# Kernel optimization log

Hardware: AMD Instinct MI355X
Metric: run time of the kernel (lower is better)

Reference implementation:

```python
import jax, jax.numpy as jnp
import numpy as np


def _patch_desc(x, patch_size):
    # x: (n, c, h, w). Replicate-pad by patch_size//2 and gather all
    # patch_size*patch_size shifted views -> (n, c*p*p, h*w) descriptors.
    n, c, h, w = x.shape
    step = patch_size // 2
    y = jnp.pad(x, ((0, 0), (0, 0), (step, step), (step, step)), mode='edge')
    feats = [y[:, :, i:i + h, j:j + w]
             for i in range(patch_size) for j in range(patch_size)]
    d = jnp.stack(feats, axis=2)            # (n, c, p*p, h, w)
    return d.reshape(n, c * patch_size * patch_size, h * w)


def setup_inputs() -> dict:
    key = jax.random.key(0)
    k1, k2 = jax.random.split(key)
    n, c, h, w = 4, 16, 64, 64
    s = jax.random.normal(k1, (n, c, h, w), dtype=jnp.float32)
    t = jax.random.normal(k2, (n, c, h, w), dtype=jnp.float32)
    return {"s": s, "t": t, "patch_size": 3}


def reference(s, t, patch_size):
    n, c, h, w = s.shape
    q = _patch_desc(s, patch_size)          # (n, d, hw) source queries
    p = _patch_desc(t, patch_size)          # (n, d, hw) target points
    # Squared-L2 nearest neighbor per source patch (exact version of FLANN kNN)
    qn = jnp.sum(q * q, axis=1)             # (n, hw)
    pn = jnp.sum(p * p, axis=1)             # (n, hw)
    cross = jnp.einsum('ndi,ndj->nij', q, p)  # (n, hw_q, hw_t)
    d2 = qn[:, :, None] - 2.0 * cross + pn[:, None, :]
    idx = jnp.argmin(d2, axis=2)            # (n, hw) flat target index
    nnd = jnp.min(d2, axis=2)               # (n, hw) squared distance
    idy = idx // w
    idx_x = idx % w
    nnf = jnp.stack([idy.reshape(n, h, w), idx_x.reshape(n, h, w)], axis=1)
    nnd = nnd.reshape(n, 1, h, w)
    return nnf.astype(jnp.int32), nnd
```

## Files before the change

kernel.cpp:

```cpp
#include <hip/hip_runtime.h>


#define N_  4
#define C_  16
#define H_  64
#define W_  64
#define HW_ 4096
#define K_  160
#define SPLITS_M 4
#define KKSTRIDE 528

#define SPLITS_V 4
#define TILES_PER_SPLIT_V 4

typedef _Float16 f16;
typedef _Float16 f16x8 __attribute__((ext_vector_type(8)));
typedef float    f32x4 __attribute__((ext_vector_type(4)));
typedef float    f32x16 __attribute__((ext_vector_type(16)));

__device__ __forceinline__ int iclamp(int v, int lo, int hi) {
    return v < lo ? lo : (v > hi ? hi : v);
}

__device__ __forceinline__ void async_ld16(const void* g, void* l) {
    __builtin_amdgcn_global_load_lds(
        (const __attribute__((address_space(1))) unsigned int*)g,
        (__attribute__((address_space(3))) unsigned int*)l, 16, 0, 0);
}

__global__ __launch_bounds__(256)
void build_desc_norms_kernel(const float* __restrict__ s,
                             const float* __restrict__ t,
                             f16* __restrict__ Qh, f16* __restrict__ Ql,
                             f16* __restrict__ Ph, f16* __restrict__ Pl,
                             float* __restrict__ pn,
                             float* __restrict__ qn) {
    const int y0  = blockIdx.x;
    const int n   = blockIdx.y;
    const int src = blockIdx.z;
    const float* img = (src ? s : t) + n * (C_ * HW_);
    f16* Dh = src ? Qh : Ph;
    f16* Dl = src ? Ql : Pl;
    float* nrm = src ? qn : pn;

    __shared__ float imgS[3][C_][W_];
    __shared__ float nS[4][W_];
    const int tid = threadIdx.x;
    #pragma unroll
    for (int k = 0; k < 12; ++k) {
        const int idx = tid + k * 256;
        const int x = idx & 63, c = (idx >> 6) & 15, r = idx >> 10;
        const int gy = iclamp(y0 + r - 1, 0, H_ - 1);
        imgS[r][c][x] = img[c * HW_ + gy * W_ + x];
    }
    __syncthreads();

    const int q = tid >> 6, x = tid & 63;
    const int pix = y0 * W_ + x;
    float nacc = 0.f;
    #pragma unroll
    for (int u = 0; u < 5; ++u) {
        const int kk = q * 5 + u;
        if (kk < 18) {
            f16x8 hv, lv;
            const int d  = kk >> 1;
            const int c0 = (kk & 1) * 8;
            const int dy = (d * 11) >> 5;
            const int dx = d - dy * 3;
            const int xs = iclamp(x + dx - 1, 0, W_ - 1);
            #pragma unroll
            for (int cc = 0; cc < 8; ++cc) {
                const float v = imgS[dy][c0 + cc][xs];
                const f16 h = (f16)v;
                hv[cc] = h;
                lv[cc] = (f16)(v - (float)h);
                nacc += v * v;
            }
            const size_t off = ((size_t)(n * 20 + kk) * HW_ + pix) * 8;
            *(f16x8*)&Dh[off] = hv;
            *(f16x8*)&Dl[off] = lv;
        }
    }
    nS[q][x] = nacc;
    __syncthreads();
    if (tid < W_)
        nrm[n * HW_ + pix] = nS[0][tid] + nS[1][tid] + nS[2][tid] + nS[3][tid];
}

__global__ __launch_bounds__(256, 2)
void mfma_nn_kernel(const f16* __restrict__ Qh, const f16* __restrict__ Ql,
                    const f16* __restrict__ Ph, const f16* __restrict__ Pl,
                    const float* __restrict__ pn_g,
                    unsigned long long* __restrict__ partial) {
    const int bid   = blockIdx.x;
    const int split = bid & 3;
    const int n     = (bid >> 2) & 3;
    const int iblk  = bid >> 4;
    const int tid  = threadIdx.x;
    const int wave = tid >> 6, lane = tid & 63;
    const int col  = lane & 31;
    const int half = lane >> 5;
    const int irow0 = iblk * 128 + wave * 32;

    __shared__ f16 B0[18 * KKSTRIDE];
    __shared__ f16 B1[18 * KKSTRIDE];
    __shared__ f16 B2[18 * KKSTRIDE];
    __shared__ float pnS[1024];

    f16x8 Ah[9], Al[9];
    #pragma unroll
    for (int c = 0; c < 9; ++c) {
        const size_t off = ((size_t)(n * 20 + 2 * c + half) * HW_ +
                            irow0 + col) * 8;
        Ah[c] = *(const f16x8*)(Qh + off);
        Al[c] = *(const f16x8*)(Ql + off);
    }

    const int jsplit0 = split * 1024;
    #pragma unroll
    for (int k = 0; k < 4; ++k)
        pnS[tid + k * 256] = pn_g[n * HW_ + jsplit0 + tid + k * 256];

    float    bd[16];
    unsigned bj[16];
    #pragma unroll
    for (int r = 0; r < 16; ++r) { bd[r] = -3.0e38f; bj[r] = 0u; }

    const int nst = (wave < 2) ? 5 : 4;
    const int kk0 = (wave < 2) ? wave * 5 : 10 + (wave - 2) * 4;
    const f16* sbase = half ? Pl : Ph;

    #define STAGE(BUF, T)                                                     \
        {   _Pragma("unroll")                                                 \
            for (int u = 0; u < 5; ++u) {                                     \
                if (u < nst) {                                                \
                    const int kk = kk0 + u;                                   \
                    const f16* g = sbase + ((size_t)(n * 20 + kk) * HW_ +     \
                                            jsplit0 + (T) * 32 + col) * 8;    \
                    async_ld16(g, (void*)&BUF[kk * KKSTRIDE + lane * 8]);     \
                }                                                             \
            }                                                                 \
        }

    #define TWAIT()                                                           \
        {   if (wave < 2) asm volatile("s_waitcnt vmcnt(5)" ::: "memory");    \
            else          asm volatile("s_waitcnt vmcnt(4)" ::: "memory");    \
            asm volatile("s_barrier" ::: "memory");                           \
        }

    #define COMPUTE(BUF, T)                                                   \
        {   const float pnv = -0.5f * pnS[(T) * 32 + col];                    \
            f32x16 Cf;                                                        \
            _Pragma("unroll")                                                 \
            for (int r = 0; r < 16; ++r) Cf[r] = pnv;                         \
            __builtin_amdgcn_s_setprio(1);                                    \
            _Pragma("unroll")                                                 \
            for (int c = 0; c < 9; ++c) {                                     \
                const int kb = (2 * c + half) * KKSTRIDE + col * 8;           \
                const f16x8 bh = *(const f16x8*)&BUF[kb];                     \
                const f16x8 bl = *(const f16x8*)&BUF[kb + 256];               \
                Cf = __builtin_amdgcn_mfma_f32_32x32x16_f16(                  \
                    Ah[c], bh, Cf, 0, 0, 0);                                  \
                Cf = __builtin_amdgcn_mfma_f32_32x32x16_f16(                  \
                    Al[c], bh, Cf, 0, 0, 0);                                  \
                Cf = __builtin_amdgcn_mfma_f32_32x32x16_f16(                  \
                    Ah[c], bl, Cf, 0, 0, 0);                                  \
            }                                                                 \
            __builtin_amdgcn_s_setprio(0);                                    \
            const unsigned jloc = (unsigned)((T) * 32 + col);                 \
            _Pragma("unroll")                                                 \
            for (int r = 0; r < 16; ++r)                                      \
                if (Cf[r] > bd[r]) { bd[r] = Cf[r]; bj[r] = jloc; }           \
        }

    STAGE(B0, 0)
    STAGE(B1, 1)
    __syncthreads();

    for (int g = 0; g < 10; ++g) {
        const int t = g * 3;
        TWAIT()
        STAGE(B2, t + 2)
        COMPUTE(B0, t)
        TWAIT()
        STAGE(B0, t + 3)
        COMPUTE(B1, t + 1)
        TWAIT()
        STAGE(B1, t + 4)
        COMPUTE(B2, t + 2)
    }
    TWAIT()
    COMPUTE(B0, 30)
    asm volatile("s_waitcnt vmcnt(0)" ::: "memory");
    asm volatile("s_barrier" ::: "memory");
    COMPUTE(B1, 31)
    #undef STAGE
    #undef TWAIT
    #undef COMPUTE

    #pragma unroll
    for (int r = 0; r < 16; ++r) {
        float    d = bd[r];
        unsigned j = (unsigned)jsplit0 + bj[r];
        #pragma unroll
        for (int off = 1; off < 32; off <<= 1) {
            const float    od = __shfl_xor(d, off, 64);
            const unsigned oj = __shfl_xor(j, off, 64);
            const bool take = (od > d) || (od == d && oj < j);
            d = take ? od : d;
            j = take ? oj : j;
        }
        if (col == 0) {
            const int i = irow0 + (r & 3) + 8 * (r >> 2) + 4 * half;
            partial[(size_t)(split * N_ + n) * HW_ + i] =
                ((unsigned long long)j << 32) |
                (unsigned long long)__float_as_uint(-2.f * d);
        }
    }
}

__global__ __launch_bounds__(256)
void finalize_mfma_kernel(const unsigned long long* __restrict__ partial,
                          const float* __restrict__ qn_g,
                          float* __restrict__ out) {
    const int id  = blockIdx.x * 256 + threadIdx.x;
    const int n   = id >> 12;
    const int pix = id & 4095;
    float    bd = 3.0e38f;
    unsigned bj = 0u;
    #pragma unroll
    for (int sp = 0; sp < SPLITS_M; ++sp) {
        const unsigned long long v = partial[(size_t)(sp * N_ + n) * HW_ + pix];
        const float    d = __uint_as_float((unsigned)(v & 0xffffffffull));
        const unsigned j = (unsigned)(v >> 32);
        const bool take = (d < bd) || (d == bd && j < bj);
        bd = take ? d : bd;
        bj = take ? j : bj;
    }
    out[n * 2 * HW_ + pix]            = (float)(bj >> 6);
    out[n * 2 * HW_ + HW_ + pix]      = (float)(bj & 63);
    out[N_ * 2 * HW_ + n * HW_ + pix] = bd + qn_g[n * HW_ + pix];
}

__global__ __launch_bounds__(256)
void prep_norms_kernel(const float* __restrict__ s,
                       const float* __restrict__ t,
                       float* __restrict__ pn,
                       float* __restrict__ qn) {
    const int gid   = blockIdx.x * 256 + threadIdx.x;
    const int which = gid >> 14;
    const int id    = gid & 16383;
    const int n     = id >> 12;
    const int pix   = id & 4095;
    const int y = pix >> 6, x = pix & 63;
    const float* base = (which ? s : t) + n * (C_ * HW_);
    float acc = 0.f;
    for (int c = 0; c < C_; ++c) {
        const float* bc = base + c * HW_;
        #pragma unroll
        for (int dy = 0; dy < 3; ++dy) {
            const float* br = bc + iclamp(y + dy - 1, 0, H_ - 1) * W_;
            #pragma unroll
            for (int dx = 0; dx < 3; ++dx) {
                float v = br[iclamp(x + dx - 1, 0, W_ - 1)];
                acc += v * v;
            }
        }
    }
    (which ? qn : pn)[id] = acc;
}

__global__ __launch_bounds__(256)
void patchmatch_main_kernel(const float* __restrict__ s,
                            const float* __restrict__ t,
                            const float* __restrict__ pn_g,
                            const float* __restrict__ qn_g,
                            unsigned long long* __restrict__ partial) {
    const int yq    = blockIdx.x;
    const int n     = blockIdx.y;
    const int split = blockIdx.z;
    const int tid  = threadIdx.x;
    const int tx   = tid & 15;
    const int ty   = tid >> 4;
    const int i0   = ty * 4;
    const int jrow = tx >> 2;
    const int jx0  = (tx & 3) * 16;

    __shared__ float qS[C_][3][68];
    __shared__ float tS[C_][6][68];
    __shared__ float qnS[W_];

    const float* sb = s + n * (C_ * HW_);
    const float* tb = t + n * (C_ * HW_);

    #pragma unroll
    for (int k = 0; k < 3; ++k) {
        const int id = tid + k * 256;
        const int sg = id & 15;
        const int c  = (id >> 4) & 15;
        const int r  = id >> 8;
        const int gr = iclamp(yq + r - 1, 0, H_ - 1);
        const float4 v = *(const float4*)&sb[c * HW_ + gr * W_ + sg * 4];
        float* dst = &qS[c][r][1 + sg * 4];
        dst[0] = v.x; dst[1] = v.y; dst[2] = v.z; dst[3] = v.w;
    }
    if (tid < 48) {
        const int c  = tid & 15;
        const int r  = tid >> 4;
        const int gr = iclamp(yq + r - 1, 0, H_ - 1);
        qS[c][r][0]  = sb[c * HW_ + gr * W_];
        qS[c][r][65] = sb[c * HW_ + gr * W_ + 63];
    }
    if (tid < W_) qnS[tid] = qn_g[n * HW_ + yq * W_ + tid];

    unsigned long long best[4] = {~0ull, ~0ull, ~0ull, ~0ull};

    for (int ytl = 0; ytl < TILES_PER_SPLIT_V; ++ytl) {
        const int yt = split * TILES_PER_SPLIT_V + ytl;
        __syncthreads();
        #pragma unroll
        for (int k = 0; k < 6; ++k) {
            const int id = tid + k * 256;
            const int sg = id & 15;
            const int c  = (id >> 4) & 15;
            const int r  = id >> 8;
            const int gr = iclamp(4 * yt + r - 1, 0, H_ - 1);
            const float4 v = *(const float4*)&tb[c * HW_ + gr * W_ + sg * 4];
            float* dst = &tS[c][r][1 + sg * 4];
            dst[0] = v.x; dst[1] = v.y; dst[2] = v.z; dst[3] = v.w;
        }
        if (tid < 96) {
            const int c  = tid & 15;
            const int r  = tid >> 4;
            const int gr = iclamp(4 * yt + r - 1, 0, H_ - 1);
            tS[c][r][0]  = tb[c * HW_ + gr * W_];
            tS[c][r][65] = tb[c * HW_ + gr * W_ + 63];
        }
        __syncthreads();

        float acc[4][16];
        #pragma unroll
        for (int a = 0; a < 4; ++a)
            #pragma unroll
            for (int b = 0; b < 16; ++b) acc[a][b] = 0.f;

        for (int c = 0; c < C_; ++c) {
            #pragma unroll
            for (int dy = 0; dy < 3; ++dy) {
                float qv[6], tv[18];
                *(float4*)&qv[0] = *(const float4*)&qS[c][dy][i0];
                *(float2*)&qv[4] = *(const float2*)&qS[c][dy][i0 + 4];
                const float* trow = &tS[c][jrow + dy][jx0];
                *(float4*)&tv[0]  = *(const float4*)&trow[0];
                *(float4*)&tv[4]  = *(const float4*)&trow[4];
                *(float4*)&tv[8]  = *(const float4*)&trow[8];
                *(float4*)&tv[12] = *(const float4*)&trow[12];
                *(float2*)&tv[16] = *(const float2*)&trow[16];
                #pragma unroll
                for (int dx = 0; dx < 3; ++dx)
                    #pragma unroll
                    for (int a = 0; a < 4; ++a)
                        #pragma unroll
                        for (int b = 0; b < 16; ++b)
                            acc[a][b] += qv[a + dx] * tv[b + dx];
            }
        }

        const int jbase = yt * 256 + jrow * W_ + jx0;
        float pnv[16];
        const float* png = &pn_g[n * HW_ + jbase];
        *(float4*)&pnv[0]  = *(const float4*)&png[0];
        *(float4*)&pnv[4]  = *(const float4*)&png[4];
        *(float4*)&pnv[8]  = *(const float4*)&png[8];
        *(float4*)&pnv[12] = *(const float4*)&png[12];
        #pragma unroll
        for (int a = 0; a < 4; ++a) {
            const float qn = qnS[i0 + a];
            #pragma unroll
            for (int b = 0; b < 16; ++b) {
                const float d2 = qn + pnv[b] - 2.f * acc[a][b];
                unsigned long long cand =
                    ((unsigned long long)__float_as_uint(d2) << 32) |
                    (unsigned)(jbase + b);
                best[a] = cand < best[a] ? cand : best[a];
            }
        }
    }

    #pragma unroll
    for (int a = 0; a < 4; ++a) {
        unsigned long long v = best[a];
        #pragma unroll
        for (int mm = 8; mm >= 1; mm >>= 1) {
            unsigned long long o = __shfl_xor(v, mm, 64);
            v = o < v ? o : v;
        }
        best[a] = v;
    }
    if (tx == 0) {
        #pragma unroll
        for (int a = 0; a < 4; ++a)
            partial[((split * N_ + n) * HW_) + yq * W_ + i0 + a] = best[a];
    }
}

__global__ __launch_bounds__(256)
void finalize_kernel(const unsigned long long* __restrict__ partial,
                     float* __restrict__ out) {
    const int id  = blockIdx.x * 256 + threadIdx.x;
    const int n   = id >> 12;
    const int pix = id & 4095;
    unsigned long long best = ~0ull;
    #pragma unroll
    for (int sp = 0; sp < SPLITS_V; ++sp) {
        unsigned long long v = partial[(sp * N_ + n) * HW_ + pix];
        best = v < best ? v : best;
    }
    const unsigned j = (unsigned)(best & 0xffffffffu);
    const float d2 = __uint_as_float((unsigned)(best >> 32));
    out[n * 2 * HW_ + pix]            = (float)(j >> 6);
    out[n * 2 * HW_ + HW_ + pix]      = (float)(j & 63);
    out[N_ * 2 * HW_ + n * HW_ + pix] = d2;
}

__global__ __launch_bounds__(256)
void patchmatch_mono_kernel(const float* __restrict__ s,
                            const float* __restrict__ t,
                            float* __restrict__ out) {
    const int yq  = blockIdx.x;
    const int n   = blockIdx.y;
    const int tid = threadIdx.x;
    const int tx  = tid & 15;
    const int ty  = tid >> 4;
    const int i0  = ty * 4;
    const int jrow = tx >> 3;
    const int jx0  = (tx & 7) * 8;

    __shared__ float qS[C_][3][68];
    __shared__ float tS[C_][4][68];
    __shared__ float pnS[HW_];
    __shared__ float qnS[W_];

    const float* sb = s + n * (C_ * HW_);
    const float* tb = t + n * (C_ * HW_);

    for (int jj = tid; jj < HW_; jj += 256) {
        const int y = jj >> 6, x = jj & 63;
        float acc = 0.f;
        for (int c = 0; c < C_; ++c) {
            const float* tc = tb + c * HW_;
            #pragma unroll
            for (int dy = 0; dy < 3; ++dy) {
                const float* tr = tc + iclamp(y + dy - 1, 0, H_ - 1) * W_;
                #pragma unroll
                for (int dx = 0; dx < 3; ++dx) {
                    float v = tr[iclamp(x + dx - 1, 0, W_ - 1)];
                    acc += v * v;
                }
            }
        }
        pnS[jj] = acc;
    }
    for (int idx = tid; idx < C_ * 3 * 66; idx += 256) {
        const int c   = idx / (3 * 66);
        const int rem = idx - c * (3 * 66);
        const int rr  = rem / 66;
        const int xi  = rem - rr * 66;
        qS[c][rr][xi] = sb[c * HW_ + iclamp(yq + rr - 1, 0, H_ - 1) * W_ +
                           iclamp(xi - 1, 0, W_ - 1)];
    }
    __syncthreads();
    if (tid < W_) {
        float acc = 0.f;
        for (int c = 0; c < C_; ++c)
            #pragma unroll
            for (int dy = 0; dy < 3; ++dy)
                #pragma unroll
                for (int dx = 0; dx < 3; ++dx) {
                    float v = qS[c][dy][tid + dx];
                    acc += v * v;
                }
        qnS[tid] = acc;
    }

    unsigned long long best[4] = {~0ull, ~0ull, ~0ull, ~0ull};
    for (int yt = 0; yt < 32; ++yt) {
        __syncthreads();
        for (int idx = tid; idx < C_ * 4 * 66; idx += 256) {
            const int c   = idx / (4 * 66);
            const int rem = idx - c * (4 * 66);
            const int rr  = rem / 66;
            const int xi  = rem - rr * 66;
            tS[c][rr][xi] = tb[c * HW_ + iclamp(2 * yt + rr - 1, 0, H_ - 1) * W_ +
                               iclamp(xi - 1, 0, W_ - 1)];
        }
        __syncthreads();

        float acc[4][8];
        #pragma unroll
        for (int a = 0; a < 4; ++a)
            #pragma unroll
            for (int b = 0; b < 8; ++b) acc[a][b] = 0.f;

        for (int c = 0; c < C_; ++c) {
            #pragma unroll
            for (int dy = 0; dy < 3; ++dy) {
                float qv[8], tv[12];
                *(float4*)&qv[0] = *(const float4*)&qS[c][dy][i0];
                *(float4*)&qv[4] = *(const float4*)&qS[c][dy][i0 + 4];
                const float* trow = &tS[c][jrow + dy][jx0];
                *(float4*)&tv[0] = *(const float4*)&trow[0];
                *(float4*)&tv[4] = *(const float4*)&trow[4];
                *(float4*)&tv[8] = *(const float4*)&trow[8];
                #pragma unroll
                for (int dx = 0; dx < 3; ++dx)
                    #pragma unroll
                    for (int a = 0; a < 4; ++a)
                        #pragma unroll
                        for (int b = 0; b < 8; ++b)
                            acc[a][b] += qv[a + dx] * tv[b + dx];
            }
        }
        const int rbase = (2 * yt + jrow) * W_ + jx0;
        #pragma unroll
        for (int a = 0; a < 4; ++a) {
            const float qn = qnS[i0 + a];
            #pragma unroll
            for (int b = 0; b < 8; ++b) {
                const int j = rbase + b;
                const float d2 = qn + pnS[j] - 2.f * acc[a][b];
                unsigned long long cand =
                    ((unsigned long long)__float_as_uint(d2) << 32) | (unsigned)j;
                best[a] = cand < best[a] ? cand : best[a];
            }
        }
    }
    #pragma unroll
    for (int a = 0; a < 4; ++a) {
        unsigned long long v = best[a];
        #pragma unroll
        for (int mm = 8; mm >= 1; mm >>= 1) {
            unsigned long long o = __shfl_xor(v, mm, 64);
            v = o < v ? o : v;
        }
        best[a] = v;
    }
    if (tx == 0) {
        #pragma unroll
        for (int a = 0; a < 4; ++a) {
            const int x = i0 + a;
            const unsigned j = (unsigned)(best[a] & 0xffffffffu);
            const float d2 = __uint_as_float((unsigned)(best[a] >> 32));
            const int pix = yq * W_ + x;
            out[n * 2 * HW_ + pix]            = (float)(j >> 6);
            out[n * 2 * HW_ + HW_ + pix]      = (float)(j & 63);
            out[N_ * 2 * HW_ + n * HW_ + pix] = d2;
        }
    }
}

extern "C" void kernel_launch(void* const* d_in, const int* in_sizes, int n_in,
                              void* d_out, int out_size, void* d_ws, size_t ws_size,
                              hipStream_t stream) {
    const float* s = (const float*)d_in[0];
    const float* t = (const float*)d_in[1];
    float* out = (float*)d_out;

    const size_t norm_b  = (size_t)N_ * HW_ * 4;
    const size_t part_b  = (size_t)SPLITS_M * N_ * HW_ * 8;
    const size_t desc_b  = (size_t)N_ * HW_ * K_ * 2;
    const size_t need_m  = 2 * norm_b + part_b + 4 * desc_b;

    if (ws_size >= need_m) {
        char* w = (char*)d_ws;
        float* pn = (float*)w;                       w += norm_b;
        float* qn = (float*)w;                       w += norm_b;
        unsigned long long* partial = (unsigned long long*)w; w += part_b;
        f16* Qh = (f16*)w;  w += desc_b;
        f16* Ql = (f16*)w;  w += desc_b;
        f16* Ph = (f16*)w;  w += desc_b;
        f16* Pl = (f16*)w;

        build_desc_norms_kernel<<<dim3(64, N_, 2), 256, 0, stream>>>(
            s, t, Qh, Ql, Ph, Pl, pn, qn);
        mfma_nn_kernel<<<512, 256, 0, stream>>>(Qh, Ql, Ph, Pl, pn, partial);
        finalize_mfma_kernel<<<64, 256, 0, stream>>>(partial, qn, out);
        return;
    }

    const size_t need_v = 2 * norm_b + (size_t)SPLITS_V * N_ * HW_ * 8;
    if (ws_size >= need_v) {
        float* pn = (float*)d_ws;
        float* qn = pn + N_ * HW_;
        unsigned long long* partial =
            (unsigned long long*)((char*)d_ws + 2 * norm_b);
        prep_norms_kernel<<<128, 256, 0, stream>>>(s, t, pn, qn);
        dim3 grid(H_, N_, SPLITS_V);
        patchmatch_main_kernel<<<grid, 256, 0, stream>>>(s, t, pn, qn, partial);
        finalize_kernel<<<64, 256, 0, stream>>>(partial, out);
        return;
    }

    dim3 grid(H_, N_);
    patchmatch_mono_kernel<<<grid, 256, 0, stream>>>(s, t, out);
}
```

Measured before the change: 125.1 us.

## Split target range eight ways and rebalance descriptor staging across waves

Doubles the number of target splits so the grid grows to 1024 blocks, and raises the launch-bounds occupancy hint from 2 to 3 blocks per CU. Descriptors are packed into 18 chunk slots instead of 20. Only 16 chunks are staged through LDS, split evenly at 4 per wave; the last chunk pair is read straight from global memory each tile. This is meant to improve CU fill and remove the uneven wave staging, at the cost of more partial results to reduce. It also adds extra global loads inside the compute phase and drops the LDS row padding, which may cause bank conflicts.

```diff
diff --git a/kernel.cpp b/kernel.cpp
--- a/kernel.cpp
+++ b/kernel.cpp
@@ -6,9 +6,9 @@
 #define H_  64
 #define W_  64
 #define HW_ 4096
-#define K_  160
-#define SPLITS_M 4
-#define KKSTRIDE 528
+#define KK_ 18
+#define SPLITS_M 8
+#define KKSTRIDE 512
 
 #define SPLITS_V 4
 #define TILES_PER_SPLIT_V 4
@@ -61,7 +61,7 @@
     #pragma unroll
     for (int u = 0; u < 5; ++u) {
         const int kk = q * 5 + u;
-        if (kk < 18) {
+        if (kk < KK_) {
             f16x8 hv, lv;
             const int d  = kk >> 1;
             const int c0 = (kk & 1) * 8;
@@ -76,7 +76,7 @@
                 lv[cc] = (f16)(v - (float)h);
                 nacc += v * v;
             }
-            const size_t off = ((size_t)(n * 20 + kk) * HW_ + pix) * 8;
+            const size_t off = ((size_t)(n * KK_ + kk) * HW_ + pix) * 8;
             *(f16x8*)&Dh[off] = hv;
             *(f16x8*)&Dl[off] = lv;
         }
@@ -87,78 +87,77 @@
         nrm[n * HW_ + pix] = nS[0][tid] + nS[1][tid] + nS[2][tid] + nS[3][tid];
 }
 
-__global__ __launch_bounds__(256, 2)
+__global__ __launch_bounds__(256, 3)
 void mfma_nn_kernel(const f16* __restrict__ Qh, const f16* __restrict__ Ql,
                     const f16* __restrict__ Ph, const f16* __restrict__ Pl,
                     const float* __restrict__ pn_g,
                     unsigned long long* __restrict__ partial) {
     const int bid   = blockIdx.x;
-    const int split = bid & 3;
-    const int n     = (bid >> 2) & 3;
-    const int iblk  = bid >> 4;
+    const int split = bid & 7;
+    const int n     = (bid >> 3) & 3;
+    const int iblk  = bid >> 5;
     const int tid  = threadIdx.x;
     const int wave = tid >> 6, lane = tid & 63;
     const int col  = lane & 31;
     const int half = lane >> 5;
     const int irow0 = iblk * 128 + wave * 32;
 
-    __shared__ f16 B0[18 * KKSTRIDE];
-    __shared__ f16 B1[18 * KKSTRIDE];
-    __shared__ f16 B2[18 * KKSTRIDE];
-    __shared__ float pnS[1024];
+    __shared__ f16 B0[16 * KKSTRIDE];
+    __shared__ f16 B1[16 * KKSTRIDE];
+    __shared__ f16 B2[16 * KKSTRIDE];
+    __shared__ float pnS[512];
 
     f16x8 Ah[9], Al[9];
     #pragma unroll
     for (int c = 0; c < 9; ++c) {
-        const size_t off = ((size_t)(n * 20 + 2 * c + half) * HW_ +
+        const size_t off = ((size_t)(n * KK_ + 2 * c + half) * HW_ +
                             irow0 + col) * 8;
         Ah[c] = *(const f16x8*)(Qh + off);
         Al[c] = *(const f16x8*)(Ql + off);
     }
 
-    const int jsplit0 = split * 1024;
-    #pragma unroll
-    for (int k = 0; k < 4; ++k)
-        pnS[tid + k * 256] = pn_g[n * HW_ + jsplit0 + tid + k * 256];
+    const int jsplit0 = split * 512;
+    pnS[tid]       = pn_g[n * HW_ + jsplit0 + tid];
+    pnS[tid + 256] = pn_g[n * HW_ + jsplit0 + tid + 256];
+
+    const f16* p8h = Ph + ((size_t)(n * KK_ + 16 + half) * HW_ + jsplit0) * 8;
+    const f16* p8l = Pl + ((size_t)(n * KK_ + 16 + half) * HW_ + jsplit0) * 8;
 
     float    bd[16];
     unsigned bj[16];
     #pragma unroll
     for (int r = 0; r < 16; ++r) { bd[r] = -3.0e38f; bj[r] = 0u; }
 
-    const int nst = (wave < 2) ? 5 : 4;
-    const int kk0 = (wave < 2) ? wave * 5 : 10 + (wave - 2) * 4;
+    const int kk0 = wave * 4;
     const f16* sbase = half ? Pl : Ph;
 
     #define STAGE(BUF, T)                                                     \
         {   _Pragma("unroll")                                                 \
-            for (int u = 0; u < 5; ++u) {                                     \
-                if (u < nst) {                                                \
-                    const int kk = kk0 + u;                                   \
-                    const f16* g = sbase + ((size_t)(n * 20 + kk) * HW_ +     \
-                                            jsplit0 + (T) * 32 + col) * 8;    \
-                    async_ld16(g, (void*)&BUF[kk * KKSTRIDE + lane * 8]);     \
-                }                                                             \
+            for (int u = 0; u < 4; ++u) {                                     \
+                const int kk = kk0 + u;                                       \
+                const f16* g = sbase + ((size_t)(n * KK_ + kk) * HW_ +        \
+                                        jsplit0 + (T) * 32 + col) * 8;        \
+                async_ld16(g, (void*)&BUF[kk * KKSTRIDE + lane * 8]);         \
             }                                                                 \
         }
 
-    #define TWAIT()                                                           \
-        {   if (wave < 2) asm volatile("s_waitcnt vmcnt(5)" ::: "memory");    \
-            else          asm volatile("s_waitcnt vmcnt(4)" ::: "memory");    \
+    #define PHASE(WN, SBUF, ST, DOST, CBUF, CT)                               \
+        {   asm volatile("s_waitcnt vmcnt(" #WN ")" ::: "memory");            \
             asm volatile("s_barrier" ::: "memory");                           \
-        }
-
-    #define COMPUTE(BUF, T)                                                   \
-        {   const float pnv = -0.5f * pnS[(T) * 32 + col];                    \
+            const int j8 = (CT) * 32 + col;                                   \
+            const f16x8 b8h = *(const f16x8*)(p8h + (size_t)j8 * 8);          \
+            const f16x8 b8l = *(const f16x8*)(p8l + (size_t)j8 * 8);          \
+            if (DOST) STAGE(SBUF, ST);                                        \
+            const float pnv = -0.5f * pnS[j8];                                \
             f32x16 Cf;                                                        \
             _Pragma("unroll")                                                 \
             for (int r = 0; r < 16; ++r) Cf[r] = pnv;                         \
             __builtin_amdgcn_s_setprio(1);                                    \
             _Pragma("unroll")                                                 \
-            for (int c = 0; c < 9; ++c) {                                     \
+            for (int c = 0; c < 8; ++c) {                                     \
                 const int kb = (2 * c + half) * KKSTRIDE + col * 8;           \
-                const f16x8 bh = *(const f16x8*)&BUF[kb];                     \
-                const f16x8 bl = *(const f16x8*)&BUF[kb + 256];               \
+                const f16x8 bh = *(const f16x8*)&CBUF[kb];                    \
+                const f16x8 bl = *(const f16x8*)&CBUF[kb + 256];              \
                 Cf = __builtin_amdgcn_mfma_f32_32x32x16_f16(                  \
                     Ah[c], bh, Cf, 0, 0, 0);                                  \
                 Cf = __builtin_amdgcn_mfma_f32_32x32x16_f16(                  \
@@ -166,37 +165,34 @@
                 Cf = __builtin_amdgcn_mfma_f32_32x32x16_f16(                  \
                     Ah[c], bl, Cf, 0, 0, 0);                                  \
             }                                                                 \
+            Cf = __builtin_amdgcn_mfma_f32_32x32x16_f16(                      \
+                Ah[8], b8h, Cf, 0, 0, 0);                                     \
+            Cf = __builtin_amdgcn_mfma_f32_32x32x16_f16(                      \
+                Al[8], b8h, Cf, 0, 0, 0);                                     \
+            Cf = __builtin_amdgcn_mfma_f32_32x32x16_f16(                      \
+                Ah[8], b8l, Cf, 0, 0, 0);                                     \
             __builtin_amdgcn_s_setprio(0);                                    \
-            const unsigned jloc = (unsigned)((T) * 32 + col);                 \
             _Pragma("unroll")                                                 \
             for (int r = 0; r < 16; ++r)                                      \
-                if (Cf[r] > bd[r]) { bd[r] = Cf[r]; bj[r] = jloc; }           \
+                if (Cf[r] > bd[r]) { bd[r] = Cf[r]; bj[r] = (unsigned)j8; }   \
         }
 
     STAGE(B0, 0)
     STAGE(B1, 1)
     __syncthreads();
 
-    for (int g = 0; g < 10; ++g) {
+    for (int g = 0; g < 4; ++g) {
         const int t = g * 3;
-        TWAIT()
-        STAGE(B2, t + 2)
-        COMPUTE(B0, t)
-        TWAIT()
-        STAGE(B0, t + 3)
-        COMPUTE(B1, t + 1)
-        TWAIT()
-        STAGE(B1, t + 4)
-        COMPUTE(B2, t + 2)
-    }
-    TWAIT()
-    COMPUTE(B0, 30)
-    asm volatile("s_waitcnt vmcnt(0)" ::: "memory");
-    asm volatile("s_barrier" ::: "memory");
-    COMPUTE(B1, 31)
+        PHASE(4, B2, t + 2, true,  B0, t)
+        PHASE(4, B0, t + 3, true,  B1, t + 1)
+        PHASE(4, B1, t + 4, true,  B2, t + 2)
+    }
+    PHASE(4, B2, 14, true,  B0, 12)
+    PHASE(4, B0, 15, true,  B1, 13)
+    PHASE(4, B1, 0,  false, B2, 14)
+    PHASE(0, B0, 0,  false, B0, 15)
     #undef STAGE
-    #undef TWAIT
-    #undef COMPUTE
+    #undef PHASE
 
     #pragma unroll
     for (int r = 0; r < 16; ++r) {
@@ -568,7 +564,7 @@
 
     const size_t norm_b  = (size_t)N_ * HW_ * 4;
     const size_t part_b  = (size_t)SPLITS_M * N_ * HW_ * 8;
-    const size_t desc_b  = (size_t)N_ * HW_ * K_ * 2;
+    const size_t desc_b  = (size_t)N_ * HW_ * KK_ * 8 * 2;
     const size_t need_m  = 2 * norm_b + part_b + 4 * desc_b;
 
     if (ws_size >= need_m) {
@@ -583,7 +579,7 @@
 
         build_desc_norms_kernel<<<dim3(64, N_, 2), 256, 0, stream>>>(
             s, t, Qh, Ql, Ph, Pl, pn, qn);
-        mfma_nn_kernel<<<512, 256, 0, stream>>>(Qh, Ql, Ph, Pl, pn, partial);
+        mfma_nn_kernel<<<1024, 256, 0, stream>>>(Qh, Ql, Ph, Pl, pn, partial);
         finalize_mfma_kernel<<<64, 256, 0, stream>>>(partial, qn, out);
         return;
     }
```

New measurement: 165.9 us. +32.6%, slower.

## Process two target tiles per MFMA step with double-buffered tile pairs

Applied to the files above, without the earlier changes.

Restructures the MFMA nearest-neighbour loop so each wave computes two 32-column target tiles per step, interleaving two independent accumulator chains. Staging changes from a triple-buffered, per-tile scheme with partial vmcnt waits to double-buffered tile pairs with full waits and half as many barriers. The descriptor layout is also compacted from 20 to 18 k-slices and the LDS row stride is changed from 528 to 512. Independent MFMA chains should hide MFMA latency and fewer barriers cut sync cost, but the full vmcnt(0) wait reduces load/compute overlap and the unpadded stride may add LDS bank conflicts.

```diff
diff --git a/kernel.cpp b/kernel.cpp
--- a/kernel.cpp
+++ b/kernel.cpp
@@ -6,9 +6,9 @@
 #define H_  64
 #define W_  64
 #define HW_ 4096
-#define K_  160
+#define KK_ 18
 #define SPLITS_M 4
-#define KKSTRIDE 528
+#define KKSTRIDE 512
 
 #define SPLITS_V 4
 #define TILES_PER_SPLIT_V 4
@@ -61,7 +61,7 @@
     #pragma unroll
     for (int u = 0; u < 5; ++u) {
         const int kk = q * 5 + u;
-        if (kk < 18) {
+        if (kk < KK_) {
             f16x8 hv, lv;
             const int d  = kk >> 1;
             const int c0 = (kk & 1) * 8;
@@ -76,7 +76,7 @@
                 lv[cc] = (f16)(v - (float)h);
                 nacc += v * v;
             }
-            const size_t off = ((size_t)(n * 20 + kk) * HW_ + pix) * 8;
+            const size_t off = ((size_t)(n * KK_ + kk) * HW_ + pix) * 8;
             *(f16x8*)&Dh[off] = hv;
             *(f16x8*)&Dl[off] = lv;
         }
@@ -102,15 +102,13 @@
     const int half = lane >> 5;
     const int irow0 = iblk * 128 + wave * 32;
 
-    __shared__ f16 B0[18 * KKSTRIDE];
-    __shared__ f16 B1[18 * KKSTRIDE];
-    __shared__ f16 B2[18 * KKSTRIDE];
+    __shared__ f16 Bbuf[4][KK_ * KKSTRIDE];
     __shared__ float pnS[1024];
 
     f16x8 Ah[9], Al[9];
     #pragma unroll
     for (int c = 0; c < 9; ++c) {
-        const size_t off = ((size_t)(n * 20 + 2 * c + half) * HW_ +
+        const size_t off = ((size_t)(n * KK_ + 2 * c + half) * HW_ +
                             irow0 + col) * 8;
         Ah[c] = *(const f16x8*)(Qh + off);
         Al[c] = *(const f16x8*)(Ql + off);
@@ -126,77 +124,81 @@
     #pragma unroll
     for (int r = 0; r < 16; ++r) { bd[r] = -3.0e38f; bj[r] = 0u; }
 
-    const int nst = (wave < 2) ? 5 : 4;
-    const int kk0 = (wave < 2) ? wave * 5 : 10 + (wave - 2) * 4;
+    const int stile = wave >> 1;
+    const int skk0  = (wave & 1) * 9;
     const f16* sbase = half ? Pl : Ph;
 
-    #define STAGE(BUF, T)                                                     \
+    #define STAGE(PAIR, T0)                                                   \
         {   _Pragma("unroll")                                                 \
-            for (int u = 0; u < 5; ++u) {                                     \
-                if (u < nst) {                                                \
-                    const int kk = kk0 + u;                                   \
-                    const f16* g = sbase + ((size_t)(n * 20 + kk) * HW_ +     \
-                                            jsplit0 + (T) * 32 + col) * 8;    \
-                    async_ld16(g, (void*)&BUF[kk * KKSTRIDE + lane * 8]);     \
-                }                                                             \
+            for (int u = 0; u < 9; ++u) {                                     \
+                const int kk = skk0 + u;                                      \
+                const f16* g = sbase + ((size_t)(n * KK_ + kk) * HW_ +        \
+                                        jsplit0 + ((T0) + stile) * 32 +       \
+                                        col) * 8;                             \
+                async_ld16(g, (void*)&Bbuf[(PAIR) * 2 + stile]                \
+                                          [kk * KKSTRIDE + lane * 8]);        \
             }                                                                 \
         }
 
-    #define TWAIT()                                                           \
-        {   if (wave < 2) asm volatile("s_waitcnt vmcnt(5)" ::: "memory");    \
-            else          asm volatile("s_waitcnt vmcnt(4)" ::: "memory");    \
+    #define BAR()                                                             \
+        {   asm volatile("s_waitcnt vmcnt(0)" ::: "memory");                  \
             asm volatile("s_barrier" ::: "memory");                           \
         }
 
-    #define COMPUTE(BUF, T)                                                   \
-        {   const float pnv = -0.5f * pnS[(T) * 32 + col];                    \
-            f32x16 Cf;                                                        \
+    #define COMPUTE2(PAIR, T0)                                                \
+        {   const int j0 = (T0) * 32 + col;                                   \
+            const float pnv0 = -0.5f * pnS[j0];                               \
+            const float pnv1 = -0.5f * pnS[j0 + 32];                          \
+            f32x16 C0, C1;                                                    \
             _Pragma("unroll")                                                 \
-            for (int r = 0; r < 16; ++r) Cf[r] = pnv;                         \
+            for (int r = 0; r < 16; ++r) { C0[r] = pnv0; C1[r] = pnv1; }      \
             __builtin_amdgcn_s_setprio(1);                                    \
             _Pragma("unroll")                                                 \
             for (int c = 0; c < 9; ++c) {                                     \
                 const int kb = (2 * c + half) * KKSTRIDE + col * 8;           \
-                const f16x8 bh = *(const f16x8*)&BUF[kb];                     \
-                const f16x8 bl = *(const f16x8*)&BUF[kb + 256];               \
-                Cf = __builtin_amdgcn_mfma_f32_32x32x16_f16(                  \
-                    Ah[c], bh, Cf, 0, 0, 0);                                  \
-                Cf = __builtin_amdgcn_mfma_f32_32x32x16_f16(                  \
-                    Al[c], bh, Cf, 0, 0, 0);                                  \
-                Cf = __builtin_amdgcn_mfma_f32_32x32x16_f16(                  \
-                    Ah[c], bl, Cf, 0, 0, 0);                                  \
+                const f16x8 bh0 = *(const f16x8*)&Bbuf[(PAIR) * 2][kb];       \
+                const f16x8 bl0 = *(const f16x8*)&Bbuf[(PAIR) * 2][kb + 256]; \
+                const f16x8 bh1 = *(const f16x8*)&Bbuf[(PAIR) * 2 + 1][kb];   \
+                const f16x8 bl1 = *(const f16x8*)&Bbuf[(PAIR) * 2 + 1]        \
+                                                      [kb + 256];             \
+                C0 = __builtin_amdgcn_mfma_f32_32x32x16_f16(                  \
+                    Ah[c], bh0, C0, 0, 0, 0);                                 \
+                C1 = __builtin_amdgcn_mfma_f32_32x32x16_f16(                  \
+                    Ah[c], bh1, C1, 0, 0, 0);                                 \
+                C0 = __builtin_amdgcn_mfma_f32_32x32x16_f16(                  \
+                    Al[c], bh0, C0, 0, 0, 0);                                 \
+                C1 = __builtin_amdgcn_mfma_f32_32x32x16_f16(                  \
+                    Al[c], bh1, C1, 0, 0, 0);                                 \
+                C0 = __builtin_amdgcn_mfma_f32_32x32x16_f16(                  \
+                    Ah[c], bl0, C0, 0, 0, 0);                                 \
+                C1 = __builtin_amdgcn_mfma_f32_32x32x16_f16(                  \
+                    Ah[c], bl1, C1, 0, 0, 0);                                 \
             }                                                                 \
             __builtin_amdgcn_s_setprio(0);                                    \
-            const unsigned jloc = (unsigned)((T) * 32 + col);                 \
             _Pragma("unroll")                                                 \
-            for (int r = 0; r < 16; ++r)                                      \
-                if (Cf[r] > bd[r]) { bd[r] = Cf[r]; bj[r] = jloc; }           \
-        }
-
-    STAGE(B0, 0)
-    STAGE(B1, 1)
+            for (int r = 0; r < 16; ++r) {                                    \
+                if (C0[r] > bd[r]) { bd[r] = C0[r]; bj[r] = (unsigned)j0; }   \
+                if (C1[r] > bd[r]) { bd[r] = C1[r];                           \
+                                     bj[r] = (unsigned)(j0 + 32); }           \
+            }                                                                 \
+        }
+
+    STAGE(0, 0)
+    asm volatile("s_waitcnt vmcnt(0)" ::: "memory");
     __syncthreads();
 
-    for (int g = 0; g < 10; ++g) {
-        const int t = g * 3;
-        TWAIT()
-        STAGE(B2, t + 2)
-        COMPUTE(B0, t)
-        TWAIT()
-        STAGE(B0, t + 3)
-        COMPUTE(B1, t + 1)
-        TWAIT()
-        STAGE(B1, t + 4)
-        COMPUTE(B2, t + 2)
-    }
-    TWAIT()
-    COMPUTE(B0, 30)
-    asm volatile("s_waitcnt vmcnt(0)" ::: "memory");
-    asm volatile("s_barrier" ::: "memory");
-    COMPUTE(B1, 31)
+    STAGE(1, 2)  COMPUTE2(0, 0)
+    for (int gg = 0; gg < 6; ++gg) {
+        const int t4 = gg * 4;
+        BAR()  STAGE(0, t4 + 4)  COMPUTE2(1, t4 + 2)
+        BAR()  STAGE(1, t4 + 6)  COMPUTE2(0, t4 + 4)
+    }
+    BAR()  STAGE(0, 28)  COMPUTE2(1, 26)
+    BAR()  STAGE(1, 30)  COMPUTE2(0, 28)
+    BAR()               COMPUTE2(1, 30)
     #undef STAGE
-    #undef TWAIT
-    #undef COMPUTE
+    #undef BAR
+    #undef COMPUTE2
 
     #pragma unroll
     for (int r = 0; r < 16; ++r) {
@@ -568,7 +570,7 @@
 
     const size_t norm_b  = (size_t)N_ * HW_ * 4;
     const size_t part_b  = (size_t)SPLITS_M * N_ * HW_ * 8;
-    const size_t desc_b  = (size_t)N_ * HW_ * K_ * 2;
+    const size_t desc_b  = (size_t)N_ * HW_ * KK_ * 8 * 2;
     const size_t need_m  = 2 * norm_b + part_b + 4 * desc_b;
 
     if (ws_size >= need_m) {
```

After: 124.4 us. About the same (-0.6%).
